# Optimization experiments

Hardware: AMD Instinct MI355X
Metric: run time of the kernel (lower is better)

The kernel has to match this reference:

```python
import jax, jax.numpy as jnp
import numpy as np
from jax import lax

B = 16384
NWIRES = 4


def _conv(x, w, b):
    # NCHW conv, stride 1, SAME padding (pad 1 for k=3)
    y = lax.conv_general_dilated(x, w, (1, 1), ((1, 1), (1, 1)),
                                 dimension_numbers=("NCHW", "OIHW", "NCHW"))
    return y + b[None, :, None, None]


def _pool2(x):
    b, c, h, w = x.shape
    return x.reshape(b, c, h // 2, 2, w // 2, 2).max(axis=(3, 5))


def _apply_1q(state, U, wire):
    # state: (B,2,2,2,2) complex; U: (B,2,2) complex
    s = jnp.moveaxis(state, wire + 1, -1)
    s = jnp.einsum("bij,b...j->b...i", U, s)
    return jnp.moveaxis(s, -1, wire + 1)


def _apply_cnot(state, c, t):
    s0 = jnp.take(state, 0, axis=c + 1)
    s1 = jnp.take(state, 1, axis=c + 1)
    ta = t + 1 if t < c else t  # target axis index after removing control axis
    s1 = jnp.flip(s1, axis=ta)
    return jnp.stack([s0, s1], axis=c + 1)


def _ry(th):
    c = jnp.cos(th / 2)
    s = jnp.sin(th / 2)
    U = jnp.stack([jnp.stack([c, -s], -1), jnp.stack([s, c], -1)], -2)
    return U.astype(jnp.complex64)


def _rz(th):
    e = jnp.exp(-0.5j * th.astype(jnp.complex64))
    z = jnp.zeros_like(e)
    return jnp.stack([jnp.stack([e, z], -1), jnp.stack([z, jnp.conj(e)], -1)], -2)


def _rx(th):
    c = jnp.cos(th / 2).astype(jnp.complex64)
    s = jnp.sin(th / 2).astype(jnp.complex64)
    return jnp.stack([jnp.stack([c, -1j * s], -1), jnp.stack([-1j * s, c], -1)], -2)


def _circuit(params):
    # params: (B, 16) -> PauliZ expvals (B, 4)
    b = params.shape[0]
    state = jnp.zeros((b, 16), jnp.complex64).at[:, 0].set(1.0).reshape(b, 2, 2, 2, 2)
    for i in range(NWIRES):
        state = _apply_1q(state, _ry(params[:, 4 * i + 0]), i)
        state = _apply_1q(state, _rz(params[:, 4 * i + 1]), i)
        state = _apply_1q(state, _rx(params[:, 4 * i + 2]), i)
        state = _apply_cnot(state, i, (i + 1) % NWIRES)
    probs = state.real ** 2 + state.imag ** 2  # (B,2,2,2,2)
    zs = []
    for i in range(NWIRES):
        p = probs.sum(axis=tuple(a for a in range(1, 5) if a != i + 1))  # (B,2)
        zs.append(p[:, 0] - p[:, 1])
    return jnp.stack(zs, axis=-1)


def setup_inputs() -> dict:
    key = jax.random.key(0)
    ks = jax.random.split(key, 12)
    d = {}
    d["x"] = jax.random.normal(ks[0], (B, 1, 28, 28), jnp.float32)
    d["conv1_w"] = jax.random.normal(ks[1], (4, 1, 3, 3), jnp.float32) * 0.3
    d["conv1_b"] = jax.random.normal(ks[2], (4,), jnp.float32) * 0.1
    d["conv2_w"] = jax.random.normal(ks[3], (4, 4, 3, 3), jnp.float32) * 0.15
    d["conv2_b"] = jax.random.normal(ks[4], (4,), jnp.float32) * 0.1
    d["pl_w"] = jax.random.normal(ks[5], (16, 196), jnp.float32) * 0.07
    d["pl_b"] = jax.random.normal(ks[6], (16,), jnp.float32) * 0.05
    d["ro_w"] = jax.random.normal(ks[7], (4, 4), jnp.float32) * 0.5
    d["ro_b"] = jax.random.normal(ks[8], (4,), jnp.float32) * 0.1
    d["bn_w"] = jnp.ones((4,), jnp.float32)
    d["bn_b"] = jnp.zeros((4,), jnp.float32)
    return d


def reference(x, conv1_w, conv1_b, conv2_w, conv2_b, pl_w, pl_b, ro_w, ro_b, bn_w, bn_b):
    h = _pool2(jax.nn.relu(_conv(x, conv1_w, conv1_b)))   # (B,4,14,14)
    h = _pool2(jax.nn.relu(_conv(h, conv2_w, conv2_b)))   # (B,4,7,7)
    flat = h.reshape(x.shape[0], -1)                      # (B,196)
    params = flat @ pl_w.T + pl_b                         # (B,16)
    z = _circuit(params)                                  # (B,4)
    out = z @ ro_w.T + ro_b                               # (B,4)
    mean = out.mean(0)
    var = out.var(0)  # biased, matches torch BN training normalization
    return (out - mean) / jnp.sqrt(var + 1e-5) * bn_w + bn_b
```

## Files before the change

### kernel.cpp

```cpp
#include <hip/hip_runtime.h>
#include <math.h>

#define BATCH 16384

__global__ __launch_bounds__(256) void qnat_fused(
    const float* __restrict__ x,
    const float* __restrict__ w1,
    const float* __restrict__ b1,
    const float* __restrict__ w2,
    const float* __restrict__ b2,
    const float* __restrict__ plw,
    const float* __restrict__ plb,
    const float* __restrict__ rw,
    const float* __restrict__ rb,
    float* __restrict__ pre,
    float* __restrict__ stats)
{
  __shared__ float s_w1[36];
  __shared__ float s_b1[4];
  __shared__ float s_w2[144];
  __shared__ float s_b2[4];
  __shared__ float xs[4][30 * 34];
  __shared__ float h1p[4][1164];
  __shared__ float h2[4][196];
  __shared__ float sc[4][2][16];
  __shared__ float s_red[8];

  const int tid = threadIdx.x;
  const int w = tid >> 6;
  const int lane = tid & 63;
  const int sample = blockIdx.x * 4 + w;

  if (tid < 144)      s_w2[tid] = w2[tid];
  else if (tid < 180) s_w1[tid - 144] = w1[tid - 144];
  else if (tid < 184) s_b1[tid - 180] = b1[tid - 180];
  else if (tid < 188) s_b2[tid - 184] = b2[tid - 184];
  else if (tid < 196) s_red[tid - 188] = 0.0f;

  {
    float2 zz = make_float2(0.f, 0.f);
    float2* xz = (float2*)&xs[w][0];
    for (int p = lane; p < 510; p += 64) xz[p] = zz;
    float2* hz = (float2*)&h1p[w][0];
    for (int p = lane; p < 582; p += 64) hz[p] = zz;
  }
  __syncthreads();

  {
    const float4* xb = (const float4*)(x + (size_t)sample * 784);
    #pragma unroll
    for (int t = 0; t < 4; t++) {
      int idx = t * 64 + lane;
      if (idx < 196) {
        float4 v = xb[idx];
        int r = idx / 7;
        int c4 = idx - r * 7;
        float* dst = &xs[w][(r + 1) * 34 + 1 + 4 * c4];
        dst[0] = v.x; dst[1] = v.y; dst[2] = v.z; dst[3] = v.w;
      }
    }
  }
  __syncthreads();

  if (lane < 56) {
    const int i = lane >> 2;
    const int q = lane & 3;
    float win[4][10];
    #pragma unroll
    for (int r = 0; r < 4; r++) {
      const float2* rp = (const float2*)&xs[w][(2 * i + r) * 34 + 8 * q];
      #pragma unroll
      for (int t = 0; t < 5; t++) {
        float2 v = rp[t];
        win[r][2 * t] = v.x; win[r][2 * t + 1] = v.y;
      }
    }
    #pragma unroll
    for (int c = 0; c < 4; c++) {
      float wv[9];
      #pragma unroll
      for (int t = 0; t < 9; t++) wv[t] = s_w1[c * 9 + t];
      const float bias = s_b1[c];
      #pragma unroll
      for (int jj = 0; jj < 4; jj++) {
        float m = 0.0f;
        #pragma unroll
        for (int py = 0; py < 2; py++)
          #pragma unroll
          for (int px = 0; px < 2; px++) {
            float a = bias;
            #pragma unroll
            for (int dy = 0; dy < 3; dy++)
              #pragma unroll
              for (int dx = 0; dx < 3; dx++)
                a = fmaf(win[py + dy][2 * jj + px + dx], wv[dy * 3 + dx], a);
            m = fmaxf(m, a);
          }
        int col = 4 * q + jj;
        if (col < 14) h1p[w][290 * c + 18 * (i + 1) + 1 + col] = m;
      }
    }
  }
  __syncthreads();

  if (lane < 56) {
    const int co = lane & 3;
    const int jh = (lane >> 2) & 1;
    const int i2 = lane >> 3;
    float acc[2][2][4];
    {
      const float bias = s_b2[co];
      #pragma unroll
      for (int py = 0; py < 2; py++)
        #pragma unroll
        for (int px = 0; px < 2; px++)
          #pragma unroll
          for (int jj = 0; jj < 4; jj++) acc[py][px][jj] = bias;
    }
    #pragma unroll
    for (int ci = 0; ci < 4; ci++) {
      float win[4][10];
      #pragma unroll
      for (int r = 0; r < 4; r++) {
        const float2* rp = (const float2*)&h1p[w][290 * ci + 18 * (2 * i2 + r) + 8 * jh];
        #pragma unroll
        for (int t = 0; t < 5; t++) {
          float2 v = rp[t];
          win[r][2 * t] = v.x; win[r][2 * t + 1] = v.y;
        }
      }
      float wv[9];
      const int wb = (co * 4 + ci) * 9;
      #pragma unroll
      for (int t = 0; t < 9; t++) wv[t] = s_w2[wb + t];
      #pragma unroll
      for (int jj = 0; jj < 4; jj++)
        #pragma unroll
        for (int py = 0; py < 2; py++)
          #pragma unroll
          for (int px = 0; px < 2; px++) {
            float a = acc[py][px][jj];
            #pragma unroll
            for (int dy = 0; dy < 3; dy++)
              #pragma unroll
              for (int dx = 0; dx < 3; dx++)
                a = fmaf(win[py + dy][2 * jj + px + dx], wv[dy * 3 + dx], a);
            acc[py][px][jj] = a;
          }
    }
    #pragma unroll
    for (int jj = 0; jj < 4; jj++) {
      int J = 4 * jh + jj;
      if (J < 7) {
        float m = fmaxf(fmaxf(acc[0][0][jj], acc[0][1][jj]),
                        fmaxf(acc[1][0][jj], acc[1][1][jj]));
        h2[w][49 * co + 7 * i2 + J] = fmaxf(m, 0.0f);
      }
    }
  }
  __syncthreads();

  {
    const int k = lane & 15;
    const int part = lane >> 4;
    const float* hh = &h2[w][part * 49];
    const float* wp = plw + k * 196 + part * 49;
    float s = 0.0f;
    #pragma unroll
    for (int f = 0; f < 49; f++) s = fmaf(hh[f], wp[f], s);
    s += __shfl_down(s, 32, 64);
    s += __shfl_down(s, 16, 64);
    if (part == 0) {
      float pv = s + plb[k];
      float sv, cv;
      __sincosf(pv * 0.5f, &sv, &cv);
      sc[w][0][k] = cv;
      sc[w][1][k] = sv;
    }
  }

  if (lane < 16) {
    const int l = lane;
    float re = (l == 0) ? 1.0f : 0.0f;
    float im = 0.0f;
    #pragma unroll
    for (int qi = 0; qi < 4; qi++) {
      const int beta = 3 - qi;
      const int m = 1 << beta;
      const int b = (l >> beta) & 1;
      float c = sc[w][0][4 * qi], s = sc[w][1][4 * qi];
      float pr_ = __shfl_xor(re, m, 64), pi_ = __shfl_xor(im, m, 64);
      float sg = b ? s : -s;
      re = fmaf(c, re, sg * pr_);
      im = fmaf(c, im, sg * pi_);
      c = sc[w][0][4 * qi + 1]; s = sc[w][1][4 * qi + 1];
      float sz = b ? s : -s;
      float nr = c * re - sz * im;
      float ni = c * im + sz * re;
      re = nr; im = ni;
      c = sc[w][0][4 * qi + 2]; s = sc[w][1][4 * qi + 2];
      pr_ = __shfl_xor(re, m, 64); pi_ = __shfl_xor(im, m, 64);
      nr = fmaf(c, re, s * pi_);
      ni = fmaf(c, im, -s * pr_);
      re = nr; im = ni;
      const int tm = 1 << (3 - ((qi + 1) & 3));
      float fr = __shfl_xor(re, tm, 64), fi = __shfl_xor(im, tm, 64);
      if (b) { re = fr; im = fi; }
    }
    float pr2 = re * re + im * im;
    float z0 = ((l >> 3) & 1) ? -pr2 : pr2;
    float z1 = ((l >> 2) & 1) ? -pr2 : pr2;
    float z2 = ((l >> 1) & 1) ? -pr2 : pr2;
    float z3 = (l & 1) ? -pr2 : pr2;
    #pragma unroll
    for (int off = 8; off >= 1; off >>= 1) {
      z0 += __shfl_xor(z0, off, 64);
      z1 += __shfl_xor(z1, off, 64);
      z2 += __shfl_xor(z2, off, 64);
      z3 += __shfl_xor(z3, off, 64);
    }
    if (l == 0) {
      float o0 = fmaf(rw[0],  z0, fmaf(rw[1],  z1, fmaf(rw[2],  z2, fmaf(rw[3],  z3, rb[0]))));
      float o1 = fmaf(rw[4],  z0, fmaf(rw[5],  z1, fmaf(rw[6],  z2, fmaf(rw[7],  z3, rb[1]))));
      float o2 = fmaf(rw[8],  z0, fmaf(rw[9],  z1, fmaf(rw[10], z2, fmaf(rw[11], z3, rb[2]))));
      float o3 = fmaf(rw[12], z0, fmaf(rw[13], z1, fmaf(rw[14], z2, fmaf(rw[15], z3, rb[3]))));
      *(float4*)(pre + (size_t)sample * 4) = make_float4(o0, o1, o2, o3);
      atomicAdd(&s_red[0], o0); atomicAdd(&s_red[4], o0 * o0);
      atomicAdd(&s_red[1], o1); atomicAdd(&s_red[5], o1 * o1);
      atomicAdd(&s_red[2], o2); atomicAdd(&s_red[6], o2 * o2);
      atomicAdd(&s_red[3], o3); atomicAdd(&s_red[7], o3 * o3);
    }
  }
  __syncthreads();
  if (tid < 8) atomicAdd(&stats[tid], s_red[tid]);
}

__global__ __launch_bounds__(256) void qnat_bn(
    float* __restrict__ pre,
    const float* __restrict__ stats,
    const float* __restrict__ bnw,
    const float* __restrict__ bnb)
{
  int idx = blockIdx.x * 256 + threadIdx.x;
  int c = idx & 3;
  float mean = stats[c] * (1.0f / BATCH);
  float ex2 = stats[4 + c] * (1.0f / BATCH);
  float var = ex2 - mean * mean;
  float inv = rsqrtf(var + 1e-5f);
  pre[idx] = (pre[idx] - mean) * inv * bnw[c] + bnb[c];
}

extern "C" void kernel_launch(void* const* d_in, const int* in_sizes, int n_in,
                              void* d_out, int out_size, void* d_ws, size_t ws_size,
                              hipStream_t stream) {
  const float* x   = (const float*)d_in[0];
  const float* w1  = (const float*)d_in[1];
  const float* b1  = (const float*)d_in[2];
  const float* w2  = (const float*)d_in[3];
  const float* b2  = (const float*)d_in[4];
  const float* plw = (const float*)d_in[5];
  const float* plb = (const float*)d_in[6];
  const float* rw  = (const float*)d_in[7];
  const float* rb  = (const float*)d_in[8];
  const float* bnw = (const float*)d_in[9];
  const float* bnb = (const float*)d_in[10];

  float* out   = (float*)d_out;
  float* stats = (float*)d_ws;

  hipMemsetAsync(stats, 0, 8 * sizeof(float), stream);
  qnat_fused<<<BATCH / 4, 256, 0, stream>>>(x, w1, b1, w2, b2, plw, plb, rw, rb, out, stats);
  qnat_bn<<<(BATCH * 4) / 256, 256, 0, stream>>>(out, stats, bnw, bnb);
}
```

Baseline: 161.6 us.

## Load conv1 input windows straight from global and drop intra-wave block barriers

The shared-memory staging buffer for the input image is removed: each lane now reads its 4x10 input window directly from global memory with float4 loads and handles border padding in registers. The conv1 output layout is re-padded to a 20-wide stride so pooled results can be written as float4. The __syncthreads between per-wave stages are dropped, since each wave touches only its own sample's data. The per-wave cos/sin values move through wave shuffles instead of shared memory, and the shared atomics for the batch statistics become per-wave slots summed at the end. Together this cuts LDS footprint and barrier count, at the cost of relying on wave-level ordering of LDS accesses and doing more global loads per lane.

```diff
diff --git a/kernel.cpp b/kernel.cpp
--- a/kernel.cpp
+++ b/kernel.cpp
@@ -16,48 +16,25 @@
     float* __restrict__ pre,
     float* __restrict__ stats)
 {
-  __shared__ float s_w1[36];
-  __shared__ float s_b1[4];
   __shared__ float s_w2[144];
-  __shared__ float s_b2[4];
-  __shared__ float xs[4][30 * 34];
-  __shared__ float h1p[4][1164];
+  __shared__ __align__(16) float h1p[4][1296];
   __shared__ float h2[4][196];
-  __shared__ float sc[4][2][16];
-  __shared__ float s_red[8];
+  __shared__ float s_red[4][8];
 
   const int tid = threadIdx.x;
   const int w = tid >> 6;
   const int lane = tid & 63;
   const int sample = blockIdx.x * 4 + w;
 
-  if (tid < 144)      s_w2[tid] = w2[tid];
-  else if (tid < 180) s_w1[tid - 144] = w1[tid - 144];
-  else if (tid < 184) s_b1[tid - 180] = b1[tid - 180];
-  else if (tid < 188) s_b2[tid - 184] = b2[tid - 184];
-  else if (tid < 196) s_red[tid - 188] = 0.0f;
+  if (tid < 144) s_w2[tid] = w2[tid];
 
   {
-    float2 zz = make_float2(0.f, 0.f);
-    float2* xz = (float2*)&xs[w][0];
-    for (int p = lane; p < 510; p += 64) xz[p] = zz;
-    float2* hz = (float2*)&h1p[w][0];
-    for (int p = lane; p < 582; p += 64) hz[p] = zz;
-  }
-  __syncthreads();
-
-  {
-    const float4* xb = (const float4*)(x + (size_t)sample * 784);
-    #pragma unroll
-    for (int t = 0; t < 4; t++) {
-      int idx = t * 64 + lane;
-      if (idx < 196) {
-        float4 v = xb[idx];
-        int r = idx / 7;
-        int c4 = idx - r * 7;
-        float* dst = &xs[w][(r + 1) * 34 + 1 + 4 * c4];
-        dst[0] = v.x; dst[1] = v.y; dst[2] = v.z; dst[3] = v.w;
-      }
+    float4 z4 = make_float4(0.f, 0.f, 0.f, 0.f);
+    float4* hz = (float4*)&h1p[w][0];
+    #pragma unroll
+    for (int t = 0; t < 6; t++) {
+      int p = t * 64 + lane;
+      if (p < 324) hz[p] = z4;
     }
   }
   __syncthreads();
@@ -65,25 +42,33 @@
   if (lane < 56) {
     const int i = lane >> 2;
     const int q = lane & 3;
+    const float* xb = x + (size_t)sample * 784;
     float win[4][10];
     #pragma unroll
     for (int r = 0; r < 4; r++) {
-      const float2* rp = (const float2*)&xs[w][(2 * i + r) * 34 + 8 * q];
-      #pragma unroll
-      for (int t = 0; t < 5; t++) {
-        float2 v = rp[t];
-        win[r][2 * t] = v.x; win[r][2 * t + 1] = v.y;
-      }
-    }
+      int row = 2 * i - 1 + r;
+      #pragma unroll
+      for (int k = 0; k < 10; k++) win[r][k] = 0.0f;
+      if (0 <= row && row < 28) {
+        const float* rp = xb + row * 28;
+        if (q > 0) win[r][0] = rp[8 * q - 1];
+        float4 a = *(const float4*)(rp + 8 * q);
+        win[r][1] = a.x; win[r][2] = a.y; win[r][3] = a.z; win[r][4] = a.w;
+        if (q < 3) {
+          float4 bb = *(const float4*)(rp + 8 * q + 4);
+          win[r][5] = bb.x; win[r][6] = bb.y; win[r][7] = bb.z; win[r][8] = bb.w;
+          win[r][9] = rp[8 * q + 8];
+        }
+      }
+    }
+    float* hb = &h1p[w][20 * (i + 1) + 4 + 4 * q];
     #pragma unroll
     for (int c = 0; c < 4; c++) {
-      float wv[9];
-      #pragma unroll
-      for (int t = 0; t < 9; t++) wv[t] = s_w1[c * 9 + t];
-      const float bias = s_b1[c];
+      const float bias = b1[c];
+      float m[4];
       #pragma unroll
       for (int jj = 0; jj < 4; jj++) {
-        float m = 0.0f;
+        float best = 0.0f;
         #pragma unroll
         for (int py = 0; py < 2; py++)
           #pragma unroll
@@ -93,73 +78,70 @@
             for (int dy = 0; dy < 3; dy++)
               #pragma unroll
               for (int dx = 0; dx < 3; dx++)
-                a = fmaf(win[py + dy][2 * jj + px + dx], wv[dy * 3 + dx], a);
-            m = fmaxf(m, a);
+                a = fmaf(win[py + dy][2 * jj + px + dx], w1[c * 9 + dy * 3 + dx], a);
+            best = fmaxf(best, a);
           }
-        int col = 4 * q + jj;
-        if (col < 14) h1p[w][290 * c + 18 * (i + 1) + 1 + col] = m;
-      }
-    }
-  }
-  __syncthreads();
+        m[jj] = best;
+      }
+      if (q < 3) *(float4*)(hb + 320 * c) = make_float4(m[0], m[1], m[2], m[3]);
+      else       *(float2*)(hb + 320 * c) = make_float2(m[0], m[1]);
+    }
+  }
 
   if (lane < 56) {
     const int co = lane & 3;
     const int jh = (lane >> 2) & 1;
     const int i2 = lane >> 3;
-    float acc[2][2][4];
-    {
-      const float bias = s_b2[co];
+    float acc[4][2][2];
+    const float bias2 = b2[co];
+    #pragma unroll
+    for (int jj = 0; jj < 4; jj++)
       #pragma unroll
       for (int py = 0; py < 2; py++)
         #pragma unroll
-        for (int px = 0; px < 2; px++)
-          #pragma unroll
-          for (int jj = 0; jj < 4; jj++) acc[py][px][jj] = bias;
-    }
+        for (int px = 0; px < 2; px++) acc[jj][py][px] = bias2;
     #pragma unroll
     for (int ci = 0; ci < 4; ci++) {
-      float win[4][10];
+      float win[4][12];
       #pragma unroll
       for (int r = 0; r < 4; r++) {
-        const float2* rp = (const float2*)&h1p[w][290 * ci + 18 * (2 * i2 + r) + 8 * jh];
-        #pragma unroll
-        for (int t = 0; t < 5; t++) {
+        const float2* rp = (const float2*)&h1p[w][320 * ci + 20 * (2 * i2 + r) + 2 + 8 * jh];
+        #pragma unroll
+        for (int t = 0; t < 6; t++) {
           float2 v = rp[t];
           win[r][2 * t] = v.x; win[r][2 * t + 1] = v.y;
         }
       }
       float wv[9];
-      const int wb = (co * 4 + ci) * 9;
-      #pragma unroll
-      for (int t = 0; t < 9; t++) wv[t] = s_w2[wb + t];
+      #pragma unroll
+      for (int t = 0; t < 9; t++) wv[t] = s_w2[(co * 4 + ci) * 9 + t];
       #pragma unroll
       for (int jj = 0; jj < 4; jj++)
         #pragma unroll
         for (int py = 0; py < 2; py++)
           #pragma unroll
           for (int px = 0; px < 2; px++) {
-            float a = acc[py][px][jj];
+            float a = acc[jj][py][px];
             #pragma unroll
             for (int dy = 0; dy < 3; dy++)
               #pragma unroll
               for (int dx = 0; dx < 3; dx++)
-                a = fmaf(win[py + dy][2 * jj + px + dx], wv[dy * 3 + dx], a);
-            acc[py][px][jj] = a;
+                a = fmaf(win[py + dy][2 * jj + 1 + px + dx], wv[dy * 3 + dx], a);
+            acc[jj][py][px] = a;
           }
     }
     #pragma unroll
     for (int jj = 0; jj < 4; jj++) {
       int J = 4 * jh + jj;
       if (J < 7) {
-        float m = fmaxf(fmaxf(acc[0][0][jj], acc[0][1][jj]),
-                        fmaxf(acc[1][0][jj], acc[1][1][jj]));
+        float m = fmaxf(fmaxf(acc[jj][0][0], acc[jj][0][1]),
+                        fmaxf(acc[jj][1][0], acc[jj][1][1]));
         h2[w][49 * co + 7 * i2 + J] = fmaxf(m, 0.0f);
       }
     }
   }
-  __syncthreads();
-
+
+  float cv = 0.0f, sv = 0.0f;
   {
     const int k = lane & 15;
     const int part = lane >> 4;
@@ -170,12 +152,9 @@
     for (int f = 0; f < 49; f++) s = fmaf(hh[f], wp[f], s);
     s += __shfl_down(s, 32, 64);
     s += __shfl_down(s, 16, 64);
-    if (part == 0) {
+    if (lane < 16) {
       float pv = s + plb[k];
-      float sv, cv;
       __sincosf(pv * 0.5f, &sv, &cv);
-      sc[w][0][k] = cv;
-      sc[w][1][k] = sv;
     }
   }
 
@@ -188,17 +167,17 @@
       const int beta = 3 - qi;
       const int m = 1 << beta;
       const int b = (l >> beta) & 1;
-      float c = sc[w][0][4 * qi], s = sc[w][1][4 * qi];
+      float c = __shfl(cv, 4 * qi, 64), s = __shfl(sv, 4 * qi, 64);
       float pr_ = __shfl_xor(re, m, 64), pi_ = __shfl_xor(im, m, 64);
       float sg = b ? s : -s;
       re = fmaf(c, re, sg * pr_);
       im = fmaf(c, im, sg * pi_);
-      c = sc[w][0][4 * qi + 1]; s = sc[w][1][4 * qi + 1];
+      c = __shfl(cv, 4 * qi + 1, 64); s = __shfl(sv, 4 * qi + 1, 64);
       float sz = b ? s : -s;
       float nr = c * re - sz * im;
       float ni = c * im + sz * re;
       re = nr; im = ni;
-      c = sc[w][0][4 * qi + 2]; s = sc[w][1][4 * qi + 2];
+      c = __shfl(cv, 4 * qi + 2, 64); s = __shfl(sv, 4 * qi + 2, 64);
       pr_ = __shfl_xor(re, m, 64); pi_ = __shfl_xor(im, m, 64);
       nr = fmaf(c, re, s * pi_);
       ni = fmaf(c, im, -s * pr_);
@@ -225,14 +204,17 @@
       float o2 = fmaf(rw[8],  z0, fmaf(rw[9],  z1, fmaf(rw[10], z2, fmaf(rw[11], z3, rb[2]))));
       float o3 = fmaf(rw[12], z0, fmaf(rw[13], z1, fmaf(rw[14], z2, fmaf(rw[15], z3, rb[3]))));
       *(float4*)(pre + (size_t)sample * 4) = make_float4(o0, o1, o2, o3);
-      atomicAdd(&s_red[0], o0); atomicAdd(&s_red[4], o0 * o0);
-      atomicAdd(&s_red[1], o1); atomicAdd(&s_red[5], o1 * o1);
-      atomicAdd(&s_red[2], o2); atomicAdd(&s_red[6], o2 * o2);
-      atomicAdd(&s_red[3], o3); atomicAdd(&s_red[7], o3 * o3);
+      s_red[w][0] = o0; s_red[w][4] = o0 * o0;
+      s_red[w][1] = o1; s_red[w][5] = o1 * o1;
+      s_red[w][2] = o2; s_red[w][6] = o2 * o2;
+      s_red[w][3] = o3; s_red[w][7] = o3 * o3;
     }
   }
   __syncthreads();
-  if (tid < 8) atomicAdd(&stats[tid], s_red[tid]);
+  if (tid < 8) {
+    float v = s_red[0][tid] + s_red[1][tid] + s_red[2][tid] + s_red[3][tid];
+    atomicAdd(&stats[tid], v);
+  }
 }
 
 __global__ __launch_bounds__(256) void qnat_bn(
```

Result: no change. 162.3 us (+0.5%).
